# Performance work log

Hardware: AMD Instinct MI355X
Metric: run time of the kernel (lower is better)

## Reference

```python
import jax, jax.numpy as jnp
import numpy as np

NEG_SLOPE = 0.2  # PyG GATConv default


def _gcn_conv(x, src, dst, ew, W, b):
    # PyG GCNConv: add self-loops (weight 1), symmetric normalization, linear, scatter-add, bias.
    n = x.shape[0]
    loop = jnp.arange(n)
    src = jnp.concatenate([src, loop])
    dst = jnp.concatenate([dst, loop])
    ew = jnp.concatenate([ew, jnp.ones((n,), x.dtype)])
    deg = jax.ops.segment_sum(ew, dst, num_segments=n)
    dinv = jnp.where(deg > 0, 1.0 / jnp.sqrt(jnp.maximum(deg, 1e-12)), 0.0)
    norm = dinv[src] * ew * dinv[dst]          # [E']
    xw = x @ W.T                                # [n, out]
    out = jax.ops.segment_sum(norm[:, None] * xw[src], dst, num_segments=n)
    return out + b


def _gat_conv(x, src, dst, W, att_src, att_dst, b, concat_heads):
    # PyG GATConv: self-loops, per-head linear, additive attention with leaky_relu,
    # softmax over incoming edges per destination node, weighted scatter-add.
    n = x.shape[0]
    heads, ch = att_src.shape[1], att_src.shape[2]
    loop = jnp.arange(n)
    src = jnp.concatenate([src, loop])
    dst = jnp.concatenate([dst, loop])
    xw = (x @ W.T).reshape(n, heads, ch)        # [n, H, C]
    a_s = (xw * att_src).sum(-1)                 # [n, H]
    a_d = (xw * att_dst).sum(-1)                 # [n, H]
    e = jax.nn.leaky_relu(a_s[src] + a_d[dst], NEG_SLOPE)  # [E', H]
    emax = jax.ops.segment_max(e, dst, num_segments=n)      # self-loops guarantee non-empty segments
    p = jnp.exp(e - emax[dst])
    denom = jax.ops.segment_sum(p, dst, num_segments=n)
    alpha = p / (denom[dst] + 1e-16)
    out = jax.ops.segment_sum(alpha[..., None] * xw[src], dst, num_segments=n)  # [n, H, C]
    out = out.reshape(n, heads * ch) if concat_heads else out.mean(axis=1)
    return out + b


def setup_inputs() -> dict:
    key = jax.random.key(0)
    ks = jax.random.split(key, 20)
    T, N, E, EL = 16, 2048, 16384, 8192
    D_IN, HID, D_OUT = 64, 128, 64
    s = 0.05
    inp = {
        "x": jax.random.normal(ks[0], (T, N, D_IN), jnp.float32),
        "edge_index": jax.random.randint(ks[1], (T, 2, E), 0, N, dtype=jnp.int64),
        "edge_attr": jax.random.uniform(ks[2], (T, E), jnp.float32),
        "edge_label_index": jax.random.randint(ks[3], (2, EL), 0, T * N, dtype=jnp.int64),
        # GCNConv params (conv1: in->hid, conv2: hid->hid)
        "conv1_w": jax.random.normal(ks[4], (HID, D_IN), jnp.float32) * s,
        "conv1_b": jnp.zeros((HID,), jnp.float32),
        "conv2_w": jax.random.normal(ks[5], (HID, HID), jnp.float32) * s,
        "conv2_b": jnp.zeros((HID,), jnp.float32),
        # GATConv gat1: in -> hid, heads=4, concat
        "gat1_w": jax.random.normal(ks[6], (4 * HID, D_IN), jnp.float32) * s,
        "gat1_att_src": jax.random.normal(ks[7], (1, 4, HID), jnp.float32) * s,
        "gat1_att_dst": jax.random.normal(ks[8], (1, 4, HID), jnp.float32) * s,
        "gat1_b": jnp.zeros((4 * HID,), jnp.float32),
        # GATConv gat2: 4*hid -> out, heads=1, no concat
        "gat2_w": jax.random.normal(ks[9], (D_OUT, 4 * HID), jnp.float32) * s,
        "gat2_att_src": jax.random.normal(ks[10], (1, 1, D_OUT), jnp.float32) * s,
        "gat2_att_dst": jax.random.normal(ks[11], (1, 1, D_OUT), jnp.float32) * s,
        "gat2_b": jnp.zeros((D_OUT,), jnp.float32),
        # fc_hop: 2*hid -> num_nodes
        "fc_hop_w": jax.random.normal(ks[12], (N, 2 * HID), jnp.float32) * s,
        "fc_hop_b": jnp.zeros((N,), jnp.float32),
    }
    return inp


def reference(x, edge_index, edge_attr, edge_label_index,
              conv1_w, conv1_b, conv2_w, conv2_b,
              gat1_w, gat1_att_src, gat1_att_dst, gat1_b,
              gat2_w, gat2_att_src, gat2_att_dst, gat2_b,
              fc_hop_w, fc_hop_b):
    T, N, _ = x.shape

    # --- per-timestep hop-count branch (x_low and x_high are mathematically identical) ---
    def hop_step(x_t, ei_t, ew_t):
        h = jax.nn.relu(_gcn_conv(x_t, ei_t[0], ei_t[1], ew_t, conv1_w, conv1_b))
        h = jax.nn.relu(_gcn_conv(h, ei_t[0], ei_t[1], ew_t, conv2_w, conv2_b))
        comb = jnp.concatenate([h, h], axis=-1)   # [x_low, x_high] with identical branches
        return comb @ fc_hop_w.T + fc_hop_b       # [N, num_nodes]

    hop_out = jax.vmap(hop_step)(x, edge_index, edge_attr)  # [T, N, N]

    # --- link-prediction branch: GAT over time-flattened node set ---
    xf = x.reshape(T * N, x.shape[-1])
    ef = edge_index.transpose(1, 0, 2).reshape(2, -1)  # [2, T*E]; node ids stay < N (as in source)
    z = jax.nn.relu(_gat_conv(xf, ef[0], ef[1], gat1_w, gat1_att_src, gat1_att_dst, gat1_b, True))
    # dropout(p=0.5) is identity in eval mode
    z = _gat_conv(z, ef[0], ef[1], gat2_w, gat2_att_src, gat2_att_dst, gat2_b, False)
    link_pred = (z[edge_label_index[0]] * z[edge_label_index[1]]).sum(axis=-1)  # [EL]
    return link_pred, hop_out
```

## Files before the change

kernel.cpp:

```cpp
#include <hip/hip_runtime.h>
#include <stdint.h>

typedef __attribute__((ext_vector_type(8))) short short8;
typedef __attribute__((ext_vector_type(4))) float f32x4;

#define T_   16
#define N_   2048
#define E_   16384
#define NT   32768
#define EALL 262144
#define EL_  8192

static __device__ __forceinline__ short f2bf(float f){
  union { float f; uint32_t u; } v; v.f = f;
  uint32_t r = (v.u + 0x7FFFu + ((v.u >> 16) & 1u)) >> 16;
  return (short)r;
}
static __device__ __forceinline__ float lrelu(float x){ return x > 0.f ? x : 0.2f*x; }

__global__ void k_zero(int* __restrict__ p, int n){
  int i = blockIdx.x*256 + threadIdx.x;
  if(i < n) p[i] = 0;
}
__global__ void k_cnt(const int* __restrict__ ei, int* __restrict__ cnt){
  int id = blockIdx.x*256 + threadIdx.x;
  if(id >= EALL) return;
  int t = id >> 14, e = id & (E_-1);
  int d = ei[t*2*E_ + E_ + e];
  atomicAdd(&cnt[t*N_ + d], 1);
}
__global__ __launch_bounds__(1024) void k_scan(const int* __restrict__ cnt, int* __restrict__ off){
  __shared__ int part[1024];
  int tid = threadIdx.x;
  int base = tid*32;
  int loc[32]; int s = 0;
#pragma unroll
  for(int i=0;i<32;i++){ loc[i] = s; s += cnt[base+i]; }
  part[tid] = s; __syncthreads();
  for(int d=1; d<1024; d<<=1){
    int v = (tid>=d) ? part[tid-d] : 0;
    __syncthreads();
    part[tid] += v;
    __syncthreads();
  }
  int pre = (tid==0) ? 0 : part[tid-1];
#pragma unroll
  for(int i=0;i<32;i++) off[base+i] = pre + loc[i];
  if(tid == 1023) off[NT] = part[1023];
}
__global__ void k_copyi(const int* __restrict__ a, int* __restrict__ b, int n){
  int i = blockIdx.x*256 + threadIdx.x;
  if(i < n) b[i] = a[i];
}
__global__ void k_fill(const int* __restrict__ ei, int* __restrict__ cur, int* __restrict__ csr){
  int id = blockIdx.x*256 + threadIdx.x;
  if(id >= EALL) return;
  int t = id >> 14, e = id & (E_-1);
  int s = ei[t*2*E_ + e];
  int d = ei[t*2*E_ + E_ + e];
  int pos = atomicAdd(&cur[t*N_ + d], 1);
  csr[pos] = (id << 11) | s;
}

__global__ void k_degg(const float* __restrict__ ew, const int* __restrict__ off,
                       const int* __restrict__ csr, float* __restrict__ dinv){
  int n = blockIdx.x*256 + threadIdx.x;
  if(n >= NT) return;
  float s = 1.0f;
  for(int k=off[n]; k<off[n+1]; k++) s += ew[csr[k] >> 11];
  dinv[n] = rsqrtf(s);
}

__global__ void k_coef(const int* __restrict__ ei, const float* __restrict__ ew,
                       const float* __restrict__ dinv, float* __restrict__ coef){
  int id = blockIdx.x*256 + threadIdx.x;
  if(id >= EALL) return;
  int t = id >> 14, e = id & (E_-1);
  int s = ei[t*2*E_ + e];
  int d = ei[t*2*E_ + E_ + e];
  coef[id] = dinv[t*N_ + s] * ew[id] * dinv[t*N_ + d];
}

template<int TM,int TN,bool PREACT,bool EBIAS,bool ERELU,bool OBF16>
__global__ __launch_bounds__(256) void gemm_bt(
    const float* __restrict__ A, const float* __restrict__ ab,
    const float* __restrict__ B, const float* __restrict__ bias,
    float* __restrict__ Cf, short* __restrict__ Cb, int K, int N)
{
  const int lane = threadIdx.x & 63;
  const int wv   = threadIdx.x >> 6;
  const int wi = wv >> 1, wj = wv & 1;
  const int q = lane >> 4, r = lane & 15;
  const int m0 = blockIdx.y * (2*TM*16) + wi * (TM*16);
  const int n0 = blockIdx.x * (2*TN*16) + wj * (TN*16);

  f32x4 acc[TM][TN];
#pragma unroll
  for(int i=0;i<TM;i++)
#pragma unroll
    for(int j=0;j<TN;j++) acc[i][j] = (f32x4){0.f,0.f,0.f,0.f};

  for(int k0=0;k0<K;k0+=32){
    const int ka = k0 + q*8;
    short8 af[TM], bfr[TN];
#pragma unroll
    for(int i=0;i<TM;i++){
      const float* p = A + (size_t)(m0 + i*16 + r)*K + ka;
      float4 u0 = *(const float4*)p;
      float4 u1 = *(const float4*)(p+4);
      float vv[8] = {u0.x,u0.y,u0.z,u0.w,u1.x,u1.y,u1.z,u1.w};
      if (PREACT){
        const float* bb = ab + ka;
        float4 b0 = *(const float4*)bb;
        float4 b1 = *(const float4*)(bb+4);
        float bv[8] = {b0.x,b0.y,b0.z,b0.w,b1.x,b1.y,b1.z,b1.w};
#pragma unroll
        for(int u=0;u<8;u++) vv[u] = fmaxf(vv[u]+bv[u], 0.f);
      }
      short8 s;
#pragma unroll
      for(int u=0;u<8;u++) s[u] = f2bf(vv[u]);
      af[i] = s;
    }
#pragma unroll
    for(int j=0;j<TN;j++){
      const float* p = B + (size_t)(n0 + j*16 + r)*K + ka;
      float4 u0 = *(const float4*)p;
      float4 u1 = *(const float4*)(p+4);
      float vv[8] = {u0.x,u0.y,u0.z,u0.w,u1.x,u1.y,u1.z,u1.w};
      short8 s;
#pragma unroll
      for(int u=0;u<8;u++) s[u] = f2bf(vv[u]);
      bfr[j] = s;
    }
#pragma unroll
    for(int i=0;i<TM;i++)
#pragma unroll
      for(int j=0;j<TN;j++)
        acc[i][j] = __builtin_amdgcn_mfma_f32_16x16x32_bf16(af[i], bfr[j], acc[i][j], 0,0,0);
  }

#pragma unroll
  for(int i=0;i<TM;i++){
#pragma unroll
    for(int j=0;j<TN;j++){
#pragma unroll
      for(int rr=0;rr<4;rr++){
        int row = m0 + i*16 + q*4 + rr;
        int col = n0 + j*16 + r;
        float v = acc[i][j][rr];
        if(EBIAS) v += bias[col];
        if(ERELU) v = fmaxf(v, 0.f);
        if(OBF16) Cb[(size_t)row*N + col] = f2bf(v);
        else      Cf[(size_t)row*N + col] = v;
      }
    }
  }
}

__global__ __launch_bounds__(256) void hop_gemm(
    const short* __restrict__ Abf, const short* __restrict__ Bbf,
    const float* __restrict__ bias, float* __restrict__ out)
{
  const int lane = threadIdx.x & 63;
  const int wv   = threadIdx.x >> 6;
  const int wi = wv >> 1, wj = wv & 1;
  const int q = lane >> 4, r = lane & 15;
  const int t  = blockIdx.z;
  const int m0 = blockIdx.y * 128 + wi * 64;
  const int n0 = blockIdx.x * 128 + wj * 64;
  const short* Ab = Abf + (size_t)t * N_ * 128;

  f32x4 acc[4][4];
#pragma unroll
  for(int i=0;i<4;i++)
#pragma unroll
    for(int j=0;j<4;j++) acc[i][j] = (f32x4){0.f,0.f,0.f,0.f};

#pragma unroll
  for(int k0=0;k0<128;k0+=32){
    const int ka = k0 + q*8;
    short8 af[4], bfr[4];
#pragma unroll
    for(int i=0;i<4;i++) af[i]  = *(const short8*)(Ab  + (size_t)(m0 + i*16 + r)*128 + ka);
#pragma unroll
    for(int j=0;j<4;j++) bfr[j] = *(const short8*)(Bbf + (size_t)(n0 + j*16 + r)*128 + ka);
#pragma unroll
    for(int i=0;i<4;i++)
#pragma unroll
      for(int j=0;j<4;j++)
        acc[i][j] = __builtin_amdgcn_mfma_f32_16x16x32_bf16(af[i], bfr[j], acc[i][j], 0,0,0);
  }

#pragma unroll
  for(int i=0;i<4;i++){
#pragma unroll
    for(int j=0;j<4;j++){
#pragma unroll
      for(int rr=0;rr<4;rr++){
        int row = m0 + i*16 + q*4 + rr;
        int col = n0 + j*16 + r;
        out[((size_t)t*N_ + row)*N_ + col] = acc[i][j][rr] + bias[col];
      }
    }
  }
}

__global__ __launch_bounds__(256) void k_prep1(const float* __restrict__ xw1,
    const float* __restrict__ atts, const float* __restrict__ attd,
    float* __restrict__ x1s, float* __restrict__ as1, float* __restrict__ ad1){
  int d = blockIdx.x;
  int tid = threadIdx.x;
  int h = tid >> 6, lane = tid & 63;
  float2 v = *(const float2*)(xw1 + (size_t)d*512 + tid*2);
  *(float2*)(x1s + (size_t)d*512 + tid*2) = v;
  int c = lane*2;
  float2 a = *(const float2*)(atts + h*128 + c);
  float2 b = *(const float2*)(attd + h*128 + c);
  float s  = v.x*a.x + v.y*a.y;
  float dd = v.x*b.x + v.y*b.y;
  for(int o=32;o;o>>=1){ s += __shfl_down(s,o); dd += __shfl_down(dd,o); }
  if(lane == 0){ as1[d*4+h] = s; ad1[d*4+h] = dd; }
}

__global__ __launch_bounds__(1024) void k_den1(
    const int* __restrict__ off, const int* __restrict__ csr,
    const float* __restrict__ as1, const float* __restrict__ ad1,
    float* __restrict__ p1s, float* __restrict__ den1){
  int d = blockIdx.x;
  int t = threadIdx.x >> 6;
  int lane = threadIdx.x & 63;
  __shared__ float sden[16][4];
  float ad[4];
#pragma unroll
  for(int h=0;h<4;h++) ad[h] = ad1[d*4+h];
  float sum[4] = {0.f,0.f,0.f,0.f};
  int key = t*N_ + d;
  int beg = off[key], end = off[key+1];
  for(int k=beg+lane; k<end; k+=64){
    int s = csr[k] & (N_-1);
#pragma unroll
    for(int h=0;h<4;h++){
      float p = expf(lrelu(as1[s*4+h] + ad[h]));
      p1s[(size_t)k*4+h] = p;
      sum[h] += p;
    }
  }
#pragma unroll
  for(int h=0;h<4;h++)
    for(int o=32;o;o>>=1) sum[h] += __shfl_down(sum[h], o);
  if(lane == 0){
#pragma unroll
    for(int h=0;h<4;h++) sden[t][h] = sum[h];
  }
  __syncthreads();
  if(threadIdx.x < 4){
    int h = threadIdx.x;
    float s = 0.f;
#pragma unroll
    for(int w=0;w<16;w++) s += sden[w][h];
    den1[d*4+h] = s + expf(lrelu(as1[d*4+h] + ad[h]));
  }
}

__global__ __launch_bounds__(1024) void k_z1g(
    const int* __restrict__ off, const int* __restrict__ csr,
    const float* __restrict__ p1s, const float* __restrict__ den1,
    const float* __restrict__ as1, const float* __restrict__ ad1,
    const float* __restrict__ x1s, float* __restrict__ xw1){
  int d = blockIdx.x;
  int grp = threadIdx.x >> 7;
  int cid = threadIdx.x & 127;
  int h = cid >> 5;
  __shared__ f32x4 red[7][128];
  f32x4 acc = (f32x4){0.f,0.f,0.f,0.f};
  for(int t=grp; t<16; t+=8){
    int key = t*N_ + d;
    int beg = off[key], end = off[key+1];
    for(int k=beg; k<end; k++){
      int s = csr[k] & (N_-1);
      float p = p1s[(size_t)k*4 + h];
      f32x4 u = *(const f32x4*)(x1s + (size_t)s*512 + cid*4);
      acc += u * p;
    }
  }
  if(grp) red[grp-1][cid] = acc;
  __syncthreads();
  if(grp == 0){
#pragma unroll
    for(int g=0; g<7; g++) acc += red[g][cid];
    float deninv = 1.f/(den1[d*4+h] + 1e-16f);
    float pself = expf(lrelu(as1[d*4+h] + ad1[d*4+h]));
    f32x4 v = *(const f32x4*)(x1s + (size_t)d*512 + cid*4);
    f32x4 o = (acc + v*pself) * deninv;
    *(f32x4*)(xw1 + (size_t)d*512 + cid*4) = o;
  }
}

__global__ __launch_bounds__(256) void k_prep2(const float* __restrict__ xw2b,
    const float* __restrict__ atts, const float* __restrict__ attd,
    const float* __restrict__ b2,
    float* __restrict__ x2s, float* __restrict__ as2, float* __restrict__ ad2){
  int d = blockIdx.x*4 + (threadIdx.x >> 6);
  int lane = threadIdx.x & 63;
  float v = xw2b[(size_t)d*64 + lane];
  x2s[(size_t)d*64 + lane] = v;
  float vb = v - b2[lane];
  float s = vb*atts[lane], dd = vb*attd[lane];
  for(int o=32;o;o>>=1){ s += __shfl_down(s,o); dd += __shfl_down(dd,o); }
  if(lane == 0){ as2[d] = s; ad2[d] = dd; }
}

__global__ __launch_bounds__(1024) void k_den2(
    const int* __restrict__ off, const int* __restrict__ csr,
    const float* __restrict__ as2, const float* __restrict__ ad2,
    float* __restrict__ p2s, float* __restrict__ den2){
  int d = blockIdx.x;
  int t = threadIdx.x >> 6;
  int lane = threadIdx.x & 63;
  __shared__ float sden[16];
  float ad = ad2[d];
  float sum = 0.f;
  int key = t*N_ + d;
  int beg = off[key], end = off[key+1];
  for(int k=beg+lane; k<end; k+=64){
    int s = csr[k] & (N_-1);
    float p = expf(lrelu(as2[s] + ad));
    p2s[k] = p;
    sum += p;
  }
  for(int o=32;o;o>>=1) sum += __shfl_down(sum, o);
  if(lane == 0) sden[t] = sum;
  __syncthreads();
  if(threadIdx.x == 0){
    float s = 0.f;
#pragma unroll
    for(int w=0;w<16;w++) s += sden[w];
    den2[d] = s + expf(lrelu(as2[d] + ad));
  }
}

__global__ __launch_bounds__(1024) void k_z2g(
    const int* __restrict__ off, const int* __restrict__ csr,
    const float* __restrict__ p2s, const float* __restrict__ den2,
    const float* __restrict__ as2, const float* __restrict__ ad2,
    const float* __restrict__ x2s, float* __restrict__ xw2b){
  int d = blockIdx.x;
  int t = threadIdx.x >> 6;
  int lane = threadIdx.x & 63;
  __shared__ float red[16][64];
  float acc = 0.f;
  int key = t*N_ + d;
  int beg = off[key], end = off[key+1];
  for(int k=beg; k<end; k++){
    int s = csr[k] & (N_-1);
    acc += p2s[k] * x2s[(size_t)s*64 + lane];
  }
  red[t][lane] = acc;
  __syncthreads();
  if(t == 0){
    float tot = 0.f;
#pragma unroll
    for(int w=0;w<16;w++) tot += red[w][lane];
    float deninv = 1.f/(den2[d] + 1e-16f);
    float pself = expf(lrelu(as2[d] + ad2[d]));
    xw2b[(size_t)d*64 + lane] = (tot + pself*x2s[(size_t)d*64 + lane]) * deninv;
  }
}

__global__ void k_linkpred(const float* __restrict__ z2, const int* __restrict__ eli,
                           float* __restrict__ out){
  int pair = blockIdx.x*4 + (threadIdx.x >> 6);
  int lane = threadIdx.x & 63;
  if(pair >= EL_) return;
  int a = eli[pair], b = eli[EL_ + pair];
  float v = z2[(size_t)a*64 + lane] * z2[(size_t)b*64 + lane];
  for(int off=32; off; off >>= 1) v += __shfl_down(v, off);
  if(lane == 0) out[pair] = v;
}

template<int F>
__global__ __launch_bounds__(F) void k_gcng(
    const float* __restrict__ coef, const float* __restrict__ dinv,
    const float* __restrict__ feats, const int* __restrict__ off,
    const int* __restrict__ csr, float* __restrict__ out){
  int node = blockIdx.x;
  int ch = threadIdx.x;
  int t = node >> 11;
  float di = dinv[node];
  float acc = di*di*feats[(size_t)node*F + ch];
  int beg = off[node], end = off[node+1];
  for(int k=beg; k<end; k++){
    int v = csr[k];
    int eid = v >> 11;
    int gs = (t << 11) | (v & (N_-1));
    acc += coef[eid]*feats[(size_t)gs*F + ch];
  }
  out[(size_t)node*F + ch] = acc;
}

__global__ void k_fcsum(const float* __restrict__ fcw, short* __restrict__ wbf){
  int id = blockIdx.x*256 + threadIdx.x;
  if(id >= N_*128) return;
  int j = id >> 7, k = id & 127;
  wbf[id] = f2bf(fcw[j*256 + k] + fcw[j*256 + 128 + k]);
}

extern "C" void kernel_launch(void* const* d_in, const int* in_sizes, int n_in,
                              void* d_out, int out_size, void* d_ws, size_t ws_size,
                              hipStream_t stream) {
  const float* x       = (const float*)d_in[0];
  const int*   ei      = (const int*)d_in[1];
  const float* eattr   = (const float*)d_in[2];
  const int*   eli     = (const int*)d_in[3];
  const float* conv1_w = (const float*)d_in[4];
  const float* conv1_b = (const float*)d_in[5];
  const float* conv2_w = (const float*)d_in[6];
  const float* conv2_b = (const float*)d_in[7];
  const float* gat1_w  = (const float*)d_in[8];
  const float* g1as    = (const float*)d_in[9];
  const float* g1ad    = (const float*)d_in[10];
  const float* gat1_b  = (const float*)d_in[11];
  const float* gat2_w  = (const float*)d_in[12];
  const float* g2as    = (const float*)d_in[13];
  const float* g2ad    = (const float*)d_in[14];
  const float* gat2_b  = (const float*)d_in[15];
  const float* fcw     = (const float*)d_in[16];
  const float* fcb     = (const float*)d_in[17];

  char* wp = (char*)d_ws;
  auto alloc = [&](size_t bytes)->void*{ void* r = wp; wp += (bytes + 255) & ~(size_t)255; return r; };
  int*   cnt   = (int*)alloc((size_t)NT*4);
  int*   off   = (int*)alloc((size_t)(NT+1)*4);
  int*   cur   = (int*)alloc((size_t)NT*4);
  int*   csr   = (int*)alloc((size_t)EALL*4);
  float* as1   = (float*)alloc((size_t)N_*4*4);
  float* ad1   = (float*)alloc((size_t)N_*4*4);
  float* den1  = (float*)alloc((size_t)N_*4*4);
  float* p1s   = (float*)alloc((size_t)EALL*4*4);
  float* x1s   = (float*)alloc((size_t)N_*512*4);
  float* xw2b  = (float*)alloc((size_t)NT*64*4);
  float* as2   = (float*)alloc((size_t)N_*4);
  float* ad2   = (float*)alloc((size_t)N_*4);
  float* den2  = (float*)alloc((size_t)N_*4);
  float* p2s   = (float*)alloc((size_t)EALL*4);
  float* x2s   = (float*)alloc((size_t)N_*64*4);
  float* dinv  = (float*)alloc((size_t)NT*4);
  float* coef  = (float*)alloc((size_t)EALL*4);
  float* accx  = (float*)alloc((size_t)NT*64*4);
  float* h1    = (float*)alloc((size_t)NT*128*4);
  float* acch  = (float*)alloc((size_t)NT*128*4);
  short* h2bf  = (short*)alloc((size_t)NT*128*2);
  short* fcsbf = (short*)alloc((size_t)N_*128*2);

  float* outf     = (float*)d_out;
  float* link_out = outf;
  float* hop_out  = outf + EL_;
  float* xw1      = hop_out;

  dim3 blk(256);

  k_zero<<<dim3(NT/256), blk, 0, stream>>>(cnt, NT);
  k_cnt<<<dim3(EALL/256), blk, 0, stream>>>(ei, cnt);
  k_scan<<<dim3(1), dim3(1024), 0, stream>>>(cnt, off);
  k_copyi<<<dim3(NT/256), blk, 0, stream>>>(off, cur, NT);
  k_fill<<<dim3(EALL/256), blk, 0, stream>>>(ei, cur, csr);
  k_degg<<<dim3(NT/256), blk, 0, stream>>>(eattr, off, csr, dinv);

  gemm_bt<4,4,false,false,false,false><<<dim3(4,256), blk, 0, stream>>>(
      x, nullptr, gat1_w, nullptr, xw1, nullptr, 64, 512);
  k_prep1<<<dim3(N_), blk, 0, stream>>>(xw1, g1as, g1ad, x1s, as1, ad1);
  k_den1<<<dim3(N_), dim3(1024), 0, stream>>>(off, csr, as1, ad1, p1s, den1);
  k_z1g<<<dim3(N_), dim3(1024), 0, stream>>>(off, csr, p1s, den1, as1, ad1, x1s, xw1);
  gemm_bt<4,2,true,true,false,false><<<dim3(1,256), blk, 0, stream>>>(
      xw1, gat1_b, gat2_w, gat2_b, xw2b, nullptr, 512, 64);
  k_prep2<<<dim3(N_/4), blk, 0, stream>>>(xw2b, g2as, g2ad, gat2_b, x2s, as2, ad2);
  k_den2<<<dim3(N_), dim3(1024), 0, stream>>>(off, csr, as2, ad2, p2s, den2);
  k_z2g<<<dim3(N_), dim3(1024), 0, stream>>>(off, csr, p2s, den2, as2, ad2, x2s, xw2b);
  k_linkpred<<<dim3(EL_/4), blk, 0, stream>>>(xw2b, eli, link_out);

  k_coef<<<dim3(EALL/256), blk, 0, stream>>>(ei, eattr, dinv, coef);
  k_gcng<64><<<dim3(NT), dim3(64), 0, stream>>>(coef, dinv, x, off, csr, accx);
  gemm_bt<4,4,false,true,true,false><<<dim3(1,256), blk, 0, stream>>>(
      accx, nullptr, conv1_w, conv1_b, h1, nullptr, 64, 128);
  k_gcng<128><<<dim3(NT), dim3(128), 0, stream>>>(coef, dinv, h1, off, csr, acch);
  gemm_bt<4,4,false,true,true,true><<<dim3(1,256), blk, 0, stream>>>(
      acch, nullptr, conv2_w, conv2_b, nullptr, h2bf, 128, 128);
  k_fcsum<<<dim3((N_*128)/256), blk, 0, stream>>>(fcw, fcsbf);
  hop_gemm<<<dim3(16,16,16), blk, 0, stream>>>(h2bf, fcsbf, fcb, hop_out);
}
```

Before: 654.6 us.

## Fuse GAT softmax denominator into aggregation kernels and merge small setup kernels

```diff
diff --git a/kernel.cpp b/kernel.cpp
--- a/kernel.cpp
+++ b/kernel.cpp
@@ -18,10 +18,18 @@
 }
 static __device__ __forceinline__ float lrelu(float x){ return x > 0.f ? x : 0.2f*x; }
 
-__global__ void k_zero(int* __restrict__ p, int n){
-  int i = blockIdx.x*256 + threadIdx.x;
-  if(i < n) p[i] = 0;
-}
+__global__ void k_init(const float* __restrict__ fcw, short* __restrict__ wbf,
+                       int* __restrict__ cnt){
+  int b = blockIdx.x;
+  if(b < 128){
+    cnt[b*256 + threadIdx.x] = 0;
+  } else {
+    int id = (b-128)*256 + threadIdx.x;
+    int j = id >> 7, k = id & 127;
+    wbf[id] = f2bf(fcw[j*256 + k] + fcw[j*256 + 128 + k]);
+  }
+}
+
 __global__ void k_cnt(const int* __restrict__ ei, int* __restrict__ cnt){
   int id = blockIdx.x*256 + threadIdx.x;
   if(id >= EALL) return;
@@ -29,7 +37,8 @@
   int d = ei[t*2*E_ + E_ + e];
   atomicAdd(&cnt[t*N_ + d], 1);
 }
-__global__ __launch_bounds__(1024) void k_scan(const int* __restrict__ cnt, int* __restrict__ off){
+__global__ __launch_bounds__(1024) void k_scan(const int* __restrict__ cnt,
+                                               int* __restrict__ off, int* __restrict__ cur){
   __shared__ int part[1024];
   int tid = threadIdx.x;
   int base = tid*32;
@@ -45,12 +54,8 @@
   }
   int pre = (tid==0) ? 0 : part[tid-1];
 #pragma unroll
-  for(int i=0;i<32;i++) off[base+i] = pre + loc[i];
+  for(int i=0;i<32;i++){ int v = pre + loc[i]; off[base+i] = v; cur[base+i] = v; }
   if(tid == 1023) off[NT] = part[1023];
-}
-__global__ void k_copyi(const int* __restrict__ a, int* __restrict__ b, int n){
-  int i = blockIdx.x*256 + threadIdx.x;
-  if(i < n) b[i] = a[i];
 }
 __global__ void k_fill(const int* __restrict__ ei, int* __restrict__ cur, int* __restrict__ csr){
   int id = blockIdx.x*256 + threadIdx.x;
@@ -223,49 +228,8 @@
   if(lane == 0){ as1[d*4+h] = s; ad1[d*4+h] = dd; }
 }
 
-__global__ __launch_bounds__(1024) void k_den1(
-    const int* __restrict__ off, const int* __restrict__ csr,
-    const float* __restrict__ as1, const float* __restrict__ ad1,
-    float* __restrict__ p1s, float* __restrict__ den1){
-  int d = blockIdx.x;
-  int t = threadIdx.x >> 6;
-  int lane = threadIdx.x & 63;
-  __shared__ float sden[16][4];
-  float ad[4];
-#pragma unroll
-  for(int h=0;h<4;h++) ad[h] = ad1[d*4+h];
-  float sum[4] = {0.f,0.f,0.f,0.f};
-  int key = t*N_ + d;
-  int beg = off[key], end = off[key+1];
-  for(int k=beg+lane; k<end; k+=64){
-    int s = csr[k] & (N_-1);
-#pragma unroll
-    for(int h=0;h<4;h++){
-      float p = expf(lrelu(as1[s*4+h] + ad[h]));
-      p1s[(size_t)k*4+h] = p;
-      sum[h] += p;
-    }
-  }
-#pragma unroll
-  for(int h=0;h<4;h++)
-    for(int o=32;o;o>>=1) sum[h] += __shfl_down(sum[h], o);
-  if(lane == 0){
-#pragma unroll
-    for(int h=0;h<4;h++) sden[t][h] = sum[h];
-  }
-  __syncthreads();
-  if(threadIdx.x < 4){
-    int h = threadIdx.x;
-    float s = 0.f;
-#pragma unroll
-    for(int w=0;w<16;w++) s += sden[w][h];
-    den1[d*4+h] = s + expf(lrelu(as1[d*4+h] + ad[h]));
-  }
-}
-
 __global__ __launch_bounds__(1024) void k_z1g(
     const int* __restrict__ off, const int* __restrict__ csr,
-    const float* __restrict__ p1s, const float* __restrict__ den1,
     const float* __restrict__ as1, const float* __restrict__ ad1,
     const float* __restrict__ x1s, float* __restrict__ xw1){
   int d = blockIdx.x;
@@ -273,24 +237,32 @@
   int cid = threadIdx.x & 127;
   int h = cid >> 5;
   __shared__ f32x4 red[7][128];
+  __shared__ float redd[8][128];
+  float adh = ad1[d*4+h];
   f32x4 acc = (f32x4){0.f,0.f,0.f,0.f};
+  float dsum = 0.f;
   for(int t=grp; t<16; t+=8){
     int key = t*N_ + d;
     int beg = off[key], end = off[key+1];
     for(int k=beg; k<end; k++){
       int s = csr[k] & (N_-1);
-      float p = p1s[(size_t)k*4 + h];
+      float p = expf(lrelu(as1[s*4+h] + adh));
+      dsum += p;
       f32x4 u = *(const f32x4*)(x1s + (size_t)s*512 + cid*4);
       acc += u * p;
     }
   }
   if(grp) red[grp-1][cid] = acc;
+  redd[grp][cid] = dsum;
   __syncthreads();
   if(grp == 0){
 #pragma unroll
     for(int g=0; g<7; g++) acc += red[g][cid];
-    float deninv = 1.f/(den1[d*4+h] + 1e-16f);
-    float pself = expf(lrelu(as1[d*4+h] + ad1[d*4+h]));
+    float den = 0.f;
+#pragma unroll
+    for(int g=0; g<8; g++) den += redd[g][cid];
+    float pself = expf(lrelu(as1[d*4+h] + adh));
+    float deninv = 1.f/(den + pself + 1e-16f);
     f32x4 v = *(const f32x4*)(x1s + (size_t)d*512 + cid*4);
     f32x4 o = (acc + v*pself) * deninv;
     *(f32x4*)(xw1 + (size_t)d*512 + cid*4) = o;
@@ -311,59 +283,34 @@
   if(lane == 0){ as2[d] = s; ad2[d] = dd; }
 }
 
-__global__ __launch_bounds__(1024) void k_den2(
-    const int* __restrict__ off, const int* __restrict__ csr,
-    const float* __restrict__ as2, const float* __restrict__ ad2,
-    float* __restrict__ p2s, float* __restrict__ den2){
-  int d = blockIdx.x;
-  int t = threadIdx.x >> 6;
-  int lane = threadIdx.x & 63;
-  __shared__ float sden[16];
-  float ad = ad2[d];
-  float sum = 0.f;
-  int key = t*N_ + d;
-  int beg = off[key], end = off[key+1];
-  for(int k=beg+lane; k<end; k+=64){
-    int s = csr[k] & (N_-1);
-    float p = expf(lrelu(as2[s] + ad));
-    p2s[k] = p;
-    sum += p;
-  }
-  for(int o=32;o;o>>=1) sum += __shfl_down(sum, o);
-  if(lane == 0) sden[t] = sum;
-  __syncthreads();
-  if(threadIdx.x == 0){
-    float s = 0.f;
-#pragma unroll
-    for(int w=0;w<16;w++) s += sden[w];
-    den2[d] = s + expf(lrelu(as2[d] + ad));
-  }
-}
-
 __global__ __launch_bounds__(1024) void k_z2g(
     const int* __restrict__ off, const int* __restrict__ csr,
-    const float* __restrict__ p2s, const float* __restrict__ den2,
     const float* __restrict__ as2, const float* __restrict__ ad2,
     const float* __restrict__ x2s, float* __restrict__ xw2b){
   int d = blockIdx.x;
   int t = threadIdx.x >> 6;
   int lane = threadIdx.x & 63;
   __shared__ float red[16][64];
-  float acc = 0.f;
+  __shared__ float redd[16];
+  float ad = ad2[d];
+  float acc = 0.f, dsum = 0.f;
   int key = t*N_ + d;
   int beg = off[key], end = off[key+1];
   for(int k=beg; k<end; k++){
     int s = csr[k] & (N_-1);
-    acc += p2s[k] * x2s[(size_t)s*64 + lane];
+    float p = expf(lrelu(as2[s] + ad));
+    dsum += p;
+    acc += p * x2s[(size_t)s*64 + lane];
   }
   red[t][lane] = acc;
+  if(lane == 0) redd[t] = dsum;
   __syncthreads();
   if(t == 0){
-    float tot = 0.f;
-#pragma unroll
-    for(int w=0;w<16;w++) tot += red[w][lane];
-    float deninv = 1.f/(den2[d] + 1e-16f);
-    float pself = expf(lrelu(as2[d] + ad2[d]));
+    float tot = 0.f, den = 0.f;
+#pragma unroll
+    for(int w=0;w<16;w++){ tot += red[w][lane]; den += redd[w]; }
+    float pself = expf(lrelu(as2[d] + ad));
+    float deninv = 1.f/(den + pself + 1e-16f);
     xw2b[(size_t)d*64 + lane] = (tot + pself*x2s[(size_t)d*64 + lane]) * deninv;
   }
 }
@@ -397,13 +344,6 @@
     acc += coef[eid]*feats[(size_t)gs*F + ch];
   }
   out[(size_t)node*F + ch] = acc;
-}
-
-__global__ void k_fcsum(const float* __restrict__ fcw, short* __restrict__ wbf){
-  int id = blockIdx.x*256 + threadIdx.x;
-  if(id >= N_*128) return;
-  int j = id >> 7, k = id & 127;
-  wbf[id] = f2bf(fcw[j*256 + k] + fcw[j*256 + 128 + k]);
 }
 
 extern "C" void kernel_launch(void* const* d_in, const int* in_sizes, int n_in,
@@ -436,14 +376,10 @@
   int*   csr   = (int*)alloc((size_t)EALL*4);
   float* as1   = (float*)alloc((size_t)N_*4*4);
   float* ad1   = (float*)alloc((size_t)N_*4*4);
-  float* den1  = (float*)alloc((size_t)N_*4*4);
-  float* p1s   = (float*)alloc((size_t)EALL*4*4);
   float* x1s   = (float*)alloc((size_t)N_*512*4);
   float* xw2b  = (float*)alloc((size_t)NT*64*4);
   float* as2   = (float*)alloc((size_t)N_*4);
   float* ad2   = (float*)alloc((size_t)N_*4);
-  float* den2  = (float*)alloc((size_t)N_*4);
-  float* p2s   = (float*)alloc((size_t)EALL*4);
   float* x2s   = (float*)alloc((size_t)N_*64*4);
   float* dinv  = (float*)alloc((size_t)NT*4);
   float* coef  = (float*)alloc((size_t)EALL*4);
@@ -460,32 +396,28 @@
 
   dim3 blk(256);
 
-  k_zero<<<dim3(NT/256), blk, 0, stream>>>(cnt, NT);
+  k_init<<<dim3(128+1024), blk, 0, stream>>>(fcw, fcsbf, cnt);
   k_cnt<<<dim3(EALL/256), blk, 0, stream>>>(ei, cnt);
-  k_scan<<<dim3(1), dim3(1024), 0, stream>>>(cnt, off);
-  k_copyi<<<dim3(NT/256), blk, 0, stream>>>(off, cur, NT);
+  k_scan<<<dim3(1), dim3(1024), 0, stream>>>(cnt, off, cur);
   k_fill<<<dim3(EALL/256), blk, 0, stream>>>(ei, cur, csr);
   k_degg<<<dim3(NT/256), blk, 0, stream>>>(eattr, off, csr, dinv);
+  k_coef<<<dim3(EALL/256), blk, 0, stream>>>(ei, eattr, dinv, coef);
 
   gemm_bt<4,4,false,false,false,false><<<dim3(4,256), blk, 0, stream>>>(
       x, nullptr, gat1_w, nullptr, xw1, nullptr, 64, 512);
   k_prep1<<<dim3(N_), blk, 0, stream>>>(xw1, g1as, g1ad, x1s, as1, ad1);
-  k_den1<<<dim3(N_), dim3(1024), 0, stream>>>(off, csr, as1, ad1, p1s, den1);
-  k_z1g<<<dim3(N_), dim3(1024), 0, stream>>>(off, csr, p1s, den1, as1, ad1, x1s, xw1);
+  k_z1g<<<dim3(N_), dim3(1024), 0, stream>>>(off, csr, as1, ad1, x1s, xw1);
   gemm_bt<4,2,true,true,false,false><<<dim3(1,256), blk, 0, stream>>>(
       xw1, gat1_b, gat2_w, gat2_b, xw2b, nullptr, 512, 64);
   k_prep2<<<dim3(N_/4), blk, 0, stream>>>(xw2b, g2as, g2ad, gat2_b, x2s, as2, ad2);
-  k_den2<<<dim3(N_), dim3(1024), 0, stream>>>(off, csr, as2, ad2, p2s, den2);
-  k_z2g<<<dim3(N_), dim3(1024), 0, stream>>>(off, csr, p2s, den2, as2, ad2, x2s, xw2b);
+  k_z2g<<<dim3(N_), dim3(1024), 0, stream>>>(off, csr, as2, ad2, x2s, xw2b);
   k_linkpred<<<dim3(EL_/4), blk, 0, stream>>>(xw2b, eli, link_out);
 
-  k_coef<<<dim3(EALL/256), blk, 0, stream>>>(ei, eattr, dinv, coef);
   k_gcng<64><<<dim3(NT), dim3(64), 0, stream>>>(coef, dinv, x, off, csr, accx);
   gemm_bt<4,4,false,true,true,false><<<dim3(1,256), blk, 0, stream>>>(
       accx, nullptr, conv1_w, conv1_b, h1, nullptr, 64, 128);
   k_gcng<128><<<dim3(NT), dim3(128), 0, stream>>>(coef, dinv, h1, off, csr, acch);
   gemm_bt<4,4,false,true,true,true><<<dim3(1,256), blk, 0, stream>>>(
       acch, nullptr, conv2_w, conv2_b, nullptr, h2bf, 128, 128);
-  k_fcsum<<<dim3((N_*128)/256), blk, 0, stream>>>(fcw, fcsbf);
   hop_gemm<<<dim3(16,16,16), blk, 0, stream>>>(h2bf, fcsbf, fcb, hop_out);
 }
```

Result: faster. 636.0 us (-2.8%).
